# Kernel optimization log

Measured on AMD Instinct MI355X. Metric: run time of the kernel, lower is better.

The kernel has to match this reference:

```python
import jax, jax.numpy as jnp
import numpy as np

B, S, D, E = 8, 1024, 768, 8
F = 4 * D  # 3072


def setup_inputs() -> dict:
    key = jax.random.key(0)
    ks = jax.random.split(key, 5)
    scale = 0.02
    x = jax.random.normal(ks[0], (B, S, D), jnp.float32)
    gate_w = jax.random.normal(ks[1], (D, E), jnp.float32) * scale
    gate_b = jnp.zeros((E,), jnp.float32)
    w1 = jax.random.normal(ks[2], (E, D, F), jnp.float32) * scale
    b1 = jnp.zeros((E, F), jnp.float32)
    w2 = jax.random.normal(ks[3], (E, F, D), jnp.float32) * scale
    b2 = jnp.zeros((E, D), jnp.float32)
    return {"x": x, "gate_w": gate_w, "gate_b": gate_b,
            "w1": w1, "b1": b1, "w2": w2, "b2": b2}


def reference(x, gate_w, gate_b, w1, b1, w2, b2):
    # x: [B, S, D] -> tokens [T, D]
    orig_shape = x.shape
    xt = x.reshape(-1, x.shape[-1])  # [T, D]
    gates = jax.nn.softmax(xt @ gate_w + gate_b, axis=-1)  # [T, E]
    # original takes topk(k=2) but only uses indices[:, 0] == argmax (top-1)
    expert_idx = jnp.argmax(gates, axis=-1)  # [T]
    # NOTE: original does NOT scale expert output by gate probability.
    out = jnp.zeros_like(xt)
    n_experts = w1.shape[0]
    for e in range(n_experts):  # small fixed expert loop
        h = jax.nn.gelu(xt @ w1[e] + b1[e], approximate=False)  # [T, F]
        y = h @ w2[e] + b2[e]  # [T, D]
        out = jnp.where((expert_idx == e)[:, None], y, out)
    return out.reshape(orig_shape)
```

## Files before the change

### kernel.cpp

```cpp
#include <hip/hip_runtime.h>
#include <hip/hip_bf16.h>
#include <cstdint>
#include <cstddef>

static constexpr int T_TOK = 8192;
static constexpr int D_DIM = 768;
static constexpr int E_NUM = 8;
static constexpr int F_DIM = 3072;
static constexpr int MAX_TILES = 72;

typedef __attribute__((ext_vector_type(8))) short short8;
typedef __attribute__((ext_vector_type(4))) float floatx4;
typedef __attribute__((ext_vector_type(8))) unsigned short ushort8v;

__device__ __forceinline__ void async16(const void* g, void* l) {
  __builtin_amdgcn_global_load_lds(
      (const __attribute__((address_space(1))) unsigned int*)g,
      (__attribute__((address_space(3))) unsigned int*)l, 16, 0, 0);
}

__device__ __forceinline__ float gelu_fast(float v) {
  float s = v * (1.5957691f + 0.071354813f * v * v);
  return v / (1.0f + __expf(-s));
}

__global__ __launch_bounds__(256)
void gate_kernel(const float* __restrict__ x, const float* __restrict__ gw,
                 const float* __restrict__ gb, int* __restrict__ expert_idx,
                 __hip_bfloat16* __restrict__ xb) {
  int gid = blockIdx.x * blockDim.x + threadIdx.x;
  int tok = gid >> 6;
  int lane = threadIdx.x & 63;
  if (tok >= T_TOK) return;
  const float* xr = x + (size_t)tok * D_DIM;
  __hip_bfloat16* xbr = xb + (size_t)tok * D_DIM;
  float acc[8];
#pragma unroll
  for (int e = 0; e < 8; e++) acc[e] = 0.f;
#pragma unroll
  for (int i = 0; i < D_DIM / 64; i++) {
    int d = lane + i * 64;
    float v = xr[d];
    xbr[d] = __float2bfloat16(v);
    const float4* g4 = (const float4*)(gw + (size_t)d * 8);
    float4 a = g4[0], b = g4[1];
    acc[0] += v * a.x; acc[1] += v * a.y; acc[2] += v * a.z; acc[3] += v * a.w;
    acc[4] += v * b.x; acc[5] += v * b.y; acc[6] += v * b.z; acc[7] += v * b.w;
  }
#pragma unroll
  for (int e = 0; e < 8; e++) {
#pragma unroll
    for (int o = 32; o > 0; o >>= 1) acc[e] += __shfl_xor(acc[e], o, 64);
  }
  if (lane == 0) {
    int best = 0;
    float bv = acc[0] + gb[0];
#pragma unroll
    for (int e = 1; e < 8; e++) {
      float v = acc[e] + gb[e];
      if (v > bv) { bv = v; best = e; }
    }
    expert_idx[tok] = best;
  }
}

__global__ __launch_bounds__(256)
void count_kernel(const int* __restrict__ expert_idx, int* __restrict__ counts) {
  __shared__ int h[E_NUM];
  if (threadIdx.x < E_NUM) h[threadIdx.x] = 0;
  __syncthreads();
  int t = blockIdx.x * blockDim.x + threadIdx.x;
  if (t < T_TOK) atomicAdd(&h[expert_idx[t]], 1);
  __syncthreads();
  if (threadIdx.x < E_NUM && h[threadIdx.x] > 0)
    atomicAdd(&counts[threadIdx.x], h[threadIdx.x]);
}

__global__ void offsets_kernel(const int* __restrict__ counts, int* __restrict__ offs,
                               int* __restrict__ meta) {
  if (threadIdx.x == 0) {
    int s = 0, tc = 0;
    for (int e = 0; e < E_NUM; e++) {
      offs[e] = s;
      int cnt = counts[e];
      for (int m = 0; m * 128 < cnt; m++) {
        meta[1 + tc] = e;
        meta[1 + MAX_TILES + tc] = m;
        tc++;
      }
      s += cnt;
    }
    offs[E_NUM] = s;
    meta[0] = tc;
  }
}

__global__ __launch_bounds__(256)
void scatter_kernel(const int* __restrict__ expert_idx, const int* __restrict__ offs,
                    int* __restrict__ fill, int* __restrict__ perm) {
  __shared__ int lcnt[E_NUM];
  __shared__ int lbase[E_NUM];
  if (threadIdx.x < E_NUM) lcnt[threadIdx.x] = 0;
  __syncthreads();
  int t = blockIdx.x * blockDim.x + threadIdx.x;
  int e = -1, rank = 0;
  if (t < T_TOK) {
    e = expert_idx[t];
    rank = atomicAdd(&lcnt[e], 1);
  }
  __syncthreads();
  if (threadIdx.x < E_NUM)
    lbase[threadIdx.x] = (lcnt[threadIdx.x] > 0)
                           ? atomicAdd(&fill[threadIdx.x], lcnt[threadIdx.x]) : 0;
  __syncthreads();
  if (t < T_TOK) perm[offs[e] + lbase[e] + rank] = t;
}

__global__ __launch_bounds__(256)
void transpose_bf16(const float* __restrict__ in, __hip_bfloat16* __restrict__ out,
                    int R, int C) {
  __shared__ float t[64][65];
  const float* src = in + (size_t)blockIdx.z * R * C;
  __hip_bfloat16* dst = out + (size_t)blockIdx.z * R * C;
  int r0 = blockIdx.y * 64, c0 = blockIdx.x * 64;
  int tx = threadIdx.x & 15;
  int ty = threadIdx.x >> 4;
#pragma unroll
  for (int p = 0; p < 4; p++) {
    int r = ty + p * 16;
    float4 v = *(const float4*)&src[(size_t)(r0 + r) * C + c0 + tx * 4];
    t[tx * 4 + 0][r] = v.x; t[tx * 4 + 1][r] = v.y;
    t[tx * 4 + 2][r] = v.z; t[tx * 4 + 3][r] = v.w;
  }
  __syncthreads();
  int j = threadIdx.x & 7;
#pragma unroll
  for (int p = 0; p < 2; p++) {
    int cc = (threadIdx.x >> 3) + p * 32;
    __align__(16) __hip_bfloat16 tmp[8];
#pragma unroll
    for (int i = 0; i < 8; i++) tmp[i] = __float2bfloat16(t[cc][j * 8 + i]);
    *(ushort8v*)&dst[(size_t)(c0 + cc) * R + r0 + j * 8] = *(const ushort8v*)tmp;
  }
}

__global__ __launch_bounds__(256)
void moe_gemm1(const __hip_bfloat16* __restrict__ A,
               const __hip_bfloat16* __restrict__ Bt,
               const float* __restrict__ bias,
               const int* __restrict__ meta,
               const int* __restrict__ offs,
               const int* __restrict__ perm,
               __hip_bfloat16* __restrict__ H) {
  constexpr int K = D_DIM, N = F_DIM;
  int g = blockIdx.x;
  int xcd = g & 7;
  int j = g >> 3;
  int mt = xcd * 9 + (j % 9);
  int nt = j / 9;
  if (mt >= meta[0]) return;
  int e = meta[1 + mt];
  int m0 = meta[1 + MAX_TILES + mt] * 128;
  int off = offs[e], cnt = offs[e + 1] - off;
  int n0 = nt * 128;

  __shared__ __align__(16) __hip_bfloat16 As[2 * 128 * 32];
  __shared__ __align__(16) __hip_bfloat16 Bs[2 * 128 * 32];

  int tid = threadIdx.x, lane = tid & 63, w = tid >> 6;
  int lr0 = w * 32 + (lane >> 2), lr1 = lr0 + 16;
  int ch = (lane & 3) ^ ((lane >> 3) & 3);

  int r0 = m0 + lr0; if (r0 > cnt - 1) r0 = cnt - 1;
  int r1 = m0 + lr1; if (r1 > cnt - 1) r1 = cnt - 1;
  const __hip_bfloat16* a0 = A + (size_t)perm[off + r0] * K + ch * 8;
  const __hip_bfloat16* a1 = A + (size_t)perm[off + r1] * K + ch * 8;
  const __hip_bfloat16* Bbase = Bt + ((size_t)e * N + n0) * K;
  const __hip_bfloat16* bp0 = Bbase + (size_t)lr0 * K + ch * 8;
  const __hip_bfloat16* bp1 = Bbase + (size_t)lr1 * K + ch * 8;

  int wr = (w >> 1) * 64, wc = (w & 1) * 64;
  int mrow = lane & 15, cq = lane >> 4;
  int aoff[4], boff[4];
#pragma unroll
  for (int i = 0; i < 4; i++) {
    int rr = wr + i * 16 + mrow;
    aoff[i] = rr * 32 + ((cq ^ ((rr >> 1) & 3)) * 8);
    int rb = wc + i * 16 + mrow;
    boff[i] = rb * 32 + ((cq ^ ((rb >> 1) & 3)) * 8);
  }

  floatx4 acc[4][4];
#pragma unroll
  for (int i = 0; i < 4; i++)
#pragma unroll
    for (int jj = 0; jj < 4; jj++) acc[i][jj] = (floatx4){0.f, 0.f, 0.f, 0.f};

  for (int kk = 0; kk < K; kk += 64) {
    __syncthreads();
#pragma unroll
    for (int ks = 0; ks < 2; ks++) {
      int ko = kk + ks * 32;
      async16(a0 + ko, &As[ks * 4096 + (w * 32) * 32]);
      async16(a1 + ko, &As[ks * 4096 + (w * 32 + 16) * 32]);
      async16(bp0 + ko, &Bs[ks * 4096 + (w * 32) * 32]);
      async16(bp1 + ko, &Bs[ks * 4096 + (w * 32 + 16) * 32]);
    }
    __syncthreads();
#pragma unroll
    for (int ks = 0; ks < 2; ks++) {
      short8 af[4], bf[4];
#pragma unroll
      for (int i = 0; i < 4; i++) af[i] = *(const short8*)&As[ks * 4096 + aoff[i]];
#pragma unroll
      for (int i = 0; i < 4; i++) bf[i] = *(const short8*)&Bs[ks * 4096 + boff[i]];
#pragma unroll
      for (int mi = 0; mi < 4; mi++)
#pragma unroll
        for (int ni = 0; ni < 4; ni++)
          acc[mi][ni] = __builtin_amdgcn_mfma_f32_16x16x32_bf16(af[mi], bf[ni], acc[mi][ni], 0, 0, 0);
    }
  }

#pragma unroll
  for (int mi = 0; mi < 4; mi++) {
    int rowl = wr + mi * 16 + (lane >> 4) * 4;
#pragma unroll
    for (int ni = 0; ni < 4; ni++) {
      int col = n0 + wc + ni * 16 + (lane & 15);
      float bia = bias[(size_t)e * N + col];
#pragma unroll
      for (int r = 0; r < 4; r++) {
        int gm = m0 + rowl + r;
        if (gm < cnt)
          H[(size_t)(off + gm) * N + col] = __float2bfloat16(gelu_fast(acc[mi][ni][r] + bia));
      }
    }
  }
}

__global__ __launch_bounds__(256)
void moe_gemm2(const __hip_bfloat16* __restrict__ A,
               const __hip_bfloat16* __restrict__ Bt,
               const float* __restrict__ bias,
               const int* __restrict__ meta,
               const int* __restrict__ offs,
               const int* __restrict__ perm,
               float* __restrict__ Out) {
  constexpr int K = F_DIM, N = D_DIM;
  int g = blockIdx.x;
  int xcd = g & 7;
  int j = g >> 3;
  int mt = xcd * 9 + (j % 9);
  int nt = j / 9;
  if (mt >= meta[0]) return;
  int e = meta[1 + mt];
  int m0 = meta[1 + MAX_TILES + mt] * 128;
  int off = offs[e], cnt = offs[e + 1] - off;
  int n0 = nt * 64;

  __shared__ __align__(16) __hip_bfloat16 As[2 * 128 * 32];
  __shared__ __align__(16) __hip_bfloat16 Bs[2 * 64 * 32];

  int tid = threadIdx.x, lane = tid & 63, w = tid >> 6;
  int lr0 = w * 32 + (lane >> 2), lr1 = lr0 + 16;
  int ch = (lane & 3) ^ ((lane >> 3) & 3);

  int r0 = m0 + lr0; if (r0 > cnt - 1) r0 = cnt - 1;
  int r1 = m0 + lr1; if (r1 > cnt - 1) r1 = cnt - 1;
  const __hip_bfloat16* a0 = A + (size_t)(off + r0) * K + ch * 8;
  const __hip_bfloat16* a1 = A + (size_t)(off + r1) * K + ch * 8;
  int br = w * 16 + (lane >> 2);
  const __hip_bfloat16* bp0 = Bt + ((size_t)e * N + n0 + br) * K + ch * 8;

  int mrow = lane & 15, cq = lane >> 4;
  int aoff[2], boff[4];
#pragma unroll
  for (int i = 0; i < 2; i++) {
    int rr = w * 32 + i * 16 + mrow;
    aoff[i] = rr * 32 + ((cq ^ ((rr >> 1) & 3)) * 8);
  }
#pragma unroll
  for (int i = 0; i < 4; i++) {
    int rb = i * 16 + mrow;
    boff[i] = rb * 32 + ((cq ^ ((rb >> 1) & 3)) * 8);
  }

  floatx4 acc[2][4];
#pragma unroll
  for (int i = 0; i < 2; i++)
#pragma unroll
    for (int jj = 0; jj < 4; jj++) acc[i][jj] = (floatx4){0.f, 0.f, 0.f, 0.f};

  for (int kk = 0; kk < K; kk += 64) {
    __syncthreads();
#pragma unroll
    for (int ks = 0; ks < 2; ks++) {
      int ko = kk + ks * 32;
      async16(a0 + ko, &As[ks * 4096 + (w * 32) * 32]);
      async16(a1 + ko, &As[ks * 4096 + (w * 32 + 16) * 32]);
      async16(bp0 + ko, &Bs[ks * 2048 + (w * 16) * 32]);
    }
    __syncthreads();
#pragma unroll
    for (int ks = 0; ks < 2; ks++) {
      short8 af[2], bf[4];
#pragma unroll
      for (int i = 0; i < 2; i++) af[i] = *(const short8*)&As[ks * 4096 + aoff[i]];
#pragma unroll
      for (int i = 0; i < 4; i++) bf[i] = *(const short8*)&Bs[ks * 2048 + boff[i]];
#pragma unroll
      for (int mi = 0; mi < 2; mi++)
#pragma unroll
        for (int ni = 0; ni < 4; ni++)
          acc[mi][ni] = __builtin_amdgcn_mfma_f32_16x16x32_bf16(af[mi], bf[ni], acc[mi][ni], 0, 0, 0);
    }
  }

#pragma unroll
  for (int mi = 0; mi < 2; mi++) {
    int rowl = w * 32 + mi * 16 + (lane >> 4) * 4;
#pragma unroll
    for (int ni = 0; ni < 4; ni++) {
      int col = n0 + ni * 16 + (lane & 15);
      float bia = bias[(size_t)e * N + col];
#pragma unroll
      for (int r = 0; r < 4; r++) {
        int gm = m0 + rowl + r;
        if (gm < cnt)
          Out[(size_t)perm[off + gm] * N + col] = acc[mi][ni][r] + bia;
      }
    }
  }
}

extern "C" void kernel_launch(void* const* d_in, const int* in_sizes, int n_in,
                              void* d_out, int out_size, void* d_ws, size_t ws_size,
                              hipStream_t stream) {
  const float* x  = (const float*)d_in[0];
  const float* gw = (const float*)d_in[1];
  const float* gb = (const float*)d_in[2];
  const float* w1 = (const float*)d_in[3];
  const float* b1 = (const float*)d_in[4];
  const float* w2 = (const float*)d_in[5];
  const float* b2 = (const float*)d_in[6];
  float* out = (float*)d_out;

  char* ws = (char*)d_ws;
  int* counts = (int*)(ws + 0);
  int* fill   = (int*)(ws + 32);
  int* offs   = (int*)(ws + 64);
  int* meta   = (int*)(ws + 128);
  int* eidx   = (int*)(ws + 1024);
  int* perm   = (int*)(ws + 1024 + 4 * T_TOK);
  size_t off = 1024 + 8 * (size_t)T_TOK;
  __hip_bfloat16* xb  = (__hip_bfloat16*)(ws + off); off += (size_t)T_TOK * D_DIM * 2;
  __hip_bfloat16* w1t = (__hip_bfloat16*)(ws + off); off += (size_t)E_NUM * D_DIM * F_DIM * 2;
  __hip_bfloat16* w2t = (__hip_bfloat16*)(ws + off); off += (size_t)E_NUM * D_DIM * F_DIM * 2;
  __hip_bfloat16* H   = (__hip_bfloat16*)(ws + off); off += (size_t)T_TOK * F_DIM * 2;

  hipMemsetAsync(d_ws, 0, 64, stream);
  gate_kernel<<<T_TOK / 4, 256, 0, stream>>>(x, gw, gb, eidx, xb);
  count_kernel<<<T_TOK / 256, 256, 0, stream>>>(eidx, counts);
  offsets_kernel<<<1, 64, 0, stream>>>(counts, offs, meta);
  scatter_kernel<<<T_TOK / 256, 256, 0, stream>>>(eidx, offs, fill, perm);
  transpose_bf16<<<dim3(F_DIM / 64, D_DIM / 64, E_NUM), 256, 0, stream>>>(w1, w1t, D_DIM, F_DIM);
  transpose_bf16<<<dim3(D_DIM / 64, F_DIM / 64, E_NUM), 256, 0, stream>>>(w2, w2t, F_DIM, D_DIM);
  moe_gemm1<<<8 * 9 * (F_DIM / 128), 256, 0, stream>>>(xb, w1t, b1, meta, offs, perm, H);
  moe_gemm2<<<8 * 9 * (D_DIM / 64), 256, 0, stream>>>(H, w2t, b2, meta, offs, perm, out);
}
```

Before: 379.9 us.

## Double-buffer LDS tiles in a unified templated MoE GEMM with 128x128 tiles

Merges both expert GEMMs into one templated kernel that double-buffers LDS, issuing async global-to-LDS loads for the next K-step while MFMAs run on the current one, with explicit vmcnt waits and barriers. The second GEMM now uses 128-wide N tiles instead of 64, halving its grid and raising per-block reuse of the A tile. The aim is to hide global load latency that was previously exposed between two syncthreads. In exchange, LDS use doubles to 64KB per block, which may reduce occupancy, and the second GEMM has fewer blocks to spread across CUs.

```diff
diff --git a/kernel.cpp b/kernel.cpp
--- a/kernel.cpp
+++ b/kernel.cpp
@@ -144,15 +144,15 @@
   }
 }
 
-__global__ __launch_bounds__(256)
-void moe_gemm1(const __hip_bfloat16* __restrict__ A,
-               const __hip_bfloat16* __restrict__ Bt,
-               const float* __restrict__ bias,
-               const int* __restrict__ meta,
-               const int* __restrict__ offs,
-               const int* __restrict__ perm,
-               __hip_bfloat16* __restrict__ H) {
-  constexpr int K = D_DIM, N = F_DIM;
+template<int K, int N, bool FIRST>
+__global__ __launch_bounds__(256)
+void moe_gemm(const __hip_bfloat16* __restrict__ A,
+              const __hip_bfloat16* __restrict__ Bt,
+              const float* __restrict__ bias,
+              const int* __restrict__ meta,
+              const int* __restrict__ offs,
+              const int* __restrict__ perm,
+              void* __restrict__ OutP) {
   int g = blockIdx.x;
   int xcd = g & 7;
   int j = g >> 3;
@@ -164,8 +164,8 @@
   int off = offs[e], cnt = offs[e + 1] - off;
   int n0 = nt * 128;
 
-  __shared__ __align__(16) __hip_bfloat16 As[2 * 128 * 32];
-  __shared__ __align__(16) __hip_bfloat16 Bs[2 * 128 * 32];
+  __shared__ __align__(16) __hip_bfloat16 As[2 * 8192];
+  __shared__ __align__(16) __hip_bfloat16 Bs[2 * 8192];
 
   int tid = threadIdx.x, lane = tid & 63, w = tid >> 6;
   int lr0 = w * 32 + (lane >> 2), lr1 = lr0 + 16;
@@ -173,8 +173,15 @@
 
   int r0 = m0 + lr0; if (r0 > cnt - 1) r0 = cnt - 1;
   int r1 = m0 + lr1; if (r1 > cnt - 1) r1 = cnt - 1;
-  const __hip_bfloat16* a0 = A + (size_t)perm[off + r0] * K + ch * 8;
-  const __hip_bfloat16* a1 = A + (size_t)perm[off + r1] * K + ch * 8;
+  const __hip_bfloat16* a0;
+  const __hip_bfloat16* a1;
+  if constexpr (FIRST) {
+    a0 = A + (size_t)perm[off + r0] * K + ch * 8;
+    a1 = A + (size_t)perm[off + r1] * K + ch * 8;
+  } else {
+    a0 = A + (size_t)(off + r0) * K + ch * 8;
+    a1 = A + (size_t)(off + r1) * K + ch * 8;
+  }
   const __hip_bfloat16* Bbase = Bt + ((size_t)e * N + n0) * K;
   const __hip_bfloat16* bp0 = Bbase + (size_t)lr0 * K + ch * 8;
   const __hip_bfloat16* bp1 = Bbase + (size_t)lr1 * K + ch * 8;
@@ -190,36 +197,54 @@
     boff[i] = rb * 32 + ((cq ^ ((rb >> 1) & 3)) * 8);
   }
 
-  floatx4 acc[4][4];
-#pragma unroll
-  for (int i = 0; i < 4; i++)
-#pragma unroll
-    for (int jj = 0; jj < 4; jj++) acc[i][jj] = (floatx4){0.f, 0.f, 0.f, 0.f};
-
-  for (int kk = 0; kk < K; kk += 64) {
-    __syncthreads();
+  auto stage = [&](int buf, int kk) {
 #pragma unroll
     for (int ks = 0; ks < 2; ks++) {
       int ko = kk + ks * 32;
-      async16(a0 + ko, &As[ks * 4096 + (w * 32) * 32]);
-      async16(a1 + ko, &As[ks * 4096 + (w * 32 + 16) * 32]);
-      async16(bp0 + ko, &Bs[ks * 4096 + (w * 32) * 32]);
-      async16(bp1 + ko, &Bs[ks * 4096 + (w * 32 + 16) * 32]);
-    }
-    __syncthreads();
+      __hip_bfloat16* la = &As[buf * 8192 + ks * 4096];
+      __hip_bfloat16* lb = &Bs[buf * 8192 + ks * 4096];
+      async16(a0 + ko, la + (w * 32) * 32);
+      async16(a1 + ko, la + (w * 32 + 16) * 32);
+      async16(bp0 + ko, lb + (w * 32) * 32);
+      async16(bp1 + ko, lb + (w * 32 + 16) * 32);
+    }
+  };
+
+  floatx4 acc[4][4];
+#pragma unroll
+  for (int i = 0; i < 4; i++)
+#pragma unroll
+    for (int jj = 0; jj < 4; jj++) acc[i][jj] = (floatx4){0.f, 0.f, 0.f, 0.f};
+
+  constexpr int NT = K / 64;
+  stage(0, 0);
+  int p = 0;
+  for (int t = 0; t < NT; ++t) {
+    if (t + 1 < NT) {
+      stage(p ^ 1, (t + 1) * 64);
+      asm volatile("s_waitcnt vmcnt(8)" ::: "memory");
+    } else {
+      asm volatile("s_waitcnt vmcnt(0)" ::: "memory");
+    }
+    __builtin_amdgcn_s_barrier();
+    __builtin_amdgcn_sched_barrier(0);
 #pragma unroll
     for (int ks = 0; ks < 2; ks++) {
-      short8 af[4], bf[4];
-#pragma unroll
-      for (int i = 0; i < 4; i++) af[i] = *(const short8*)&As[ks * 4096 + aoff[i]];
-#pragma unroll
-      for (int i = 0; i < 4; i++) bf[i] = *(const short8*)&Bs[ks * 4096 + boff[i]];
+      int lb = p * 8192 + ks * 4096;
+      short8 af[4], bfv[4];
+#pragma unroll
+      for (int i = 0; i < 4; i++) af[i] = *(const short8*)&As[lb + aoff[i]];
+#pragma unroll
+      for (int i = 0; i < 4; i++) bfv[i] = *(const short8*)&Bs[lb + boff[i]];
 #pragma unroll
       for (int mi = 0; mi < 4; mi++)
 #pragma unroll
         for (int ni = 0; ni < 4; ni++)
-          acc[mi][ni] = __builtin_amdgcn_mfma_f32_16x16x32_bf16(af[mi], bf[ni], acc[mi][ni], 0, 0, 0);
-    }
+          acc[mi][ni] = __builtin_amdgcn_mfma_f32_16x16x32_bf16(af[mi], bfv[ni], acc[mi][ni], 0, 0, 0);
+    }
+    __builtin_amdgcn_sched_barrier(0);
+    __builtin_amdgcn_s_barrier();
+    p ^= 1;
   }
 
 #pragma unroll
@@ -232,103 +257,14 @@
 #pragma unroll
       for (int r = 0; r < 4; r++) {
         int gm = m0 + rowl + r;
-        if (gm < cnt)
-          H[(size_t)(off + gm) * N + col] = __float2bfloat16(gelu_fast(acc[mi][ni][r] + bia));
-      }
-    }
-  }
-}
-
-__global__ __launch_bounds__(256)
-void moe_gemm2(const __hip_bfloat16* __restrict__ A,
-               const __hip_bfloat16* __restrict__ Bt,
-               const float* __restrict__ bias,
-               const int* __restrict__ meta,
-               const int* __restrict__ offs,
-               const int* __restrict__ perm,
-               float* __restrict__ Out) {
-  constexpr int K = F_DIM, N = D_DIM;
-  int g = blockIdx.x;
-  int xcd = g & 7;
-  int j = g >> 3;
-  int mt = xcd * 9 + (j % 9);
-  int nt = j / 9;
-  if (mt >= meta[0]) return;
-  int e = meta[1 + mt];
-  int m0 = meta[1 + MAX_TILES + mt] * 128;
-  int off = offs[e], cnt = offs[e + 1] - off;
-  int n0 = nt * 64;
-
-  __shared__ __align__(16) __hip_bfloat16 As[2 * 128 * 32];
-  __shared__ __align__(16) __hip_bfloat16 Bs[2 * 64 * 32];
-
-  int tid = threadIdx.x, lane = tid & 63, w = tid >> 6;
-  int lr0 = w * 32 + (lane >> 2), lr1 = lr0 + 16;
-  int ch = (lane & 3) ^ ((lane >> 3) & 3);
-
-  int r0 = m0 + lr0; if (r0 > cnt - 1) r0 = cnt - 1;
-  int r1 = m0 + lr1; if (r1 > cnt - 1) r1 = cnt - 1;
-  const __hip_bfloat16* a0 = A + (size_t)(off + r0) * K + ch * 8;
-  const __hip_bfloat16* a1 = A + (size_t)(off + r1) * K + ch * 8;
-  int br = w * 16 + (lane >> 2);
-  const __hip_bfloat16* bp0 = Bt + ((size_t)e * N + n0 + br) * K + ch * 8;
-
-  int mrow = lane & 15, cq = lane >> 4;
-  int aoff[2], boff[4];
-#pragma unroll
-  for (int i = 0; i < 2; i++) {
-    int rr = w * 32 + i * 16 + mrow;
-    aoff[i] = rr * 32 + ((cq ^ ((rr >> 1) & 3)) * 8);
-  }
-#pragma unroll
-  for (int i = 0; i < 4; i++) {
-    int rb = i * 16 + mrow;
-    boff[i] = rb * 32 + ((cq ^ ((rb >> 1) & 3)) * 8);
-  }
-
-  floatx4 acc[2][4];
-#pragma unroll
-  for (int i = 0; i < 2; i++)
-#pragma unroll
-    for (int jj = 0; jj < 4; jj++) acc[i][jj] = (floatx4){0.f, 0.f, 0.f, 0.f};
-
-  for (int kk = 0; kk < K; kk += 64) {
-    __syncthreads();
-#pragma unroll
-    for (int ks = 0; ks < 2; ks++) {
-      int ko = kk + ks * 32;
-      async16(a0 + ko, &As[ks * 4096 + (w * 32) * 32]);
-      async16(a1 + ko, &As[ks * 4096 + (w * 32 + 16) * 32]);
-      async16(bp0 + ko, &Bs[ks * 2048 + (w * 16) * 32]);
-    }
-    __syncthreads();
-#pragma unroll
-    for (int ks = 0; ks < 2; ks++) {
-      short8 af[2], bf[4];
-#pragma unroll
-      for (int i = 0; i < 2; i++) af[i] = *(const short8*)&As[ks * 4096 + aoff[i]];
-#pragma unroll
-      for (int i = 0; i < 4; i++) bf[i] = *(const short8*)&Bs[ks * 2048 + boff[i]];
-#pragma unroll
-      for (int mi = 0; mi < 2; mi++)
-#pragma unroll
-        for (int ni = 0; ni < 4; ni++)
-          acc[mi][ni] = __builtin_amdgcn_mfma_f32_16x16x32_bf16(af[mi], bf[ni], acc[mi][ni], 0, 0, 0);
-    }
-  }
-
-#pragma unroll
-  for (int mi = 0; mi < 2; mi++) {
-    int rowl = w * 32 + mi * 16 + (lane >> 4) * 4;
-#pragma unroll
-    for (int ni = 0; ni < 4; ni++) {
-      int col = n0 + ni * 16 + (lane & 15);
-      float bia = bias[(size_t)e * N + col];
-#pragma unroll
-      for (int r = 0; r < 4; r++) {
-        int gm = m0 + rowl + r;
-        if (gm < cnt)
-          Out[(size_t)perm[off + gm] * N + col] = acc[mi][ni][r] + bia;
+        if (gm < cnt) {
+          if constexpr (FIRST) {
+            ((__hip_bfloat16*)OutP)[(size_t)(off + gm) * N + col] =
+                __float2bfloat16(gelu_fast(acc[mi][ni][r] + bia));
+          } else {
+            ((float*)OutP)[(size_t)perm[off + gm] * N + col] = acc[mi][ni][r] + bia;
+          }
+        }
       }
     }
   }
@@ -366,6 +302,8 @@
   scatter_kernel<<<T_TOK / 256, 256, 0, stream>>>(eidx, offs, fill, perm);
   transpose_bf16<<<dim3(F_DIM / 64, D_DIM / 64, E_NUM), 256, 0, stream>>>(w1, w1t, D_DIM, F_DIM);
   transpose_bf16<<<dim3(D_DIM / 64, F_DIM / 64, E_NUM), 256, 0, stream>>>(w2, w2t, F_DIM, D_DIM);
-  moe_gemm1<<<8 * 9 * (F_DIM / 128), 256, 0, stream>>>(xb, w1t, b1, meta, offs, perm, H);
-  moe_gemm2<<<8 * 9 * (D_DIM / 64), 256, 0, stream>>>(H, w2t, b2, meta, offs, perm, out);
-}
+  moe_gemm<D_DIM, F_DIM, true><<<8 * 9 * (F_DIM / 128), 256, 0, stream>>>(
+      xb, w1t, b1, meta, offs, perm, (void*)H);
+  moe_gemm<F_DIM, D_DIM, false><<<8 * 9 * (D_DIM / 128), 256, 0, stream>>>(
+      H, w2t, b2, meta, offs, perm, (void*)out);
+}
```

Measured after the change: 385.2 us. Within noise of the previous version (+1.4%).

## Triple-buffer gemm1 K-loop with async prefetch and fuse expert counting into gate

Applied to the files above, without the earlier changes.

The gemm1 K loop moves from a load-then-compute scheme, with two syncs per 64-wide step, to a three-slot ring of 32-wide stages. Loads are issued two stages ahead and gated by explicit vmcnt waits, so global-to-LDS transfers overlap MFMA work. Separately, per-block expert histogram counting moves into the gate kernel, which removes one kernel launch. The risks are a larger LDS footprint, and manual waitcnt values that depend on the compiler not issuing other vector memory ops in between.

```diff
diff --git a/kernel.cpp b/kernel.cpp
--- a/kernel.cpp
+++ b/kernel.cpp
@@ -27,11 +27,13 @@
 __global__ __launch_bounds__(256)
 void gate_kernel(const float* __restrict__ x, const float* __restrict__ gw,
                  const float* __restrict__ gb, int* __restrict__ expert_idx,
-                 __hip_bfloat16* __restrict__ xb) {
+                 __hip_bfloat16* __restrict__ xb, int* __restrict__ counts) {
+  __shared__ int h[E_NUM];
+  if (threadIdx.x < E_NUM) h[threadIdx.x] = 0;
+  __syncthreads();
   int gid = blockIdx.x * blockDim.x + threadIdx.x;
   int tok = gid >> 6;
   int lane = threadIdx.x & 63;
-  if (tok >= T_TOK) return;
   const float* xr = x + (size_t)tok * D_DIM;
   __hip_bfloat16* xbr = xb + (size_t)tok * D_DIM;
   float acc[8];
@@ -61,16 +63,8 @@
       if (v > bv) { bv = v; best = e; }
     }
     expert_idx[tok] = best;
-  }
-}
-
-__global__ __launch_bounds__(256)
-void count_kernel(const int* __restrict__ expert_idx, int* __restrict__ counts) {
-  __shared__ int h[E_NUM];
-  if (threadIdx.x < E_NUM) h[threadIdx.x] = 0;
-  __syncthreads();
-  int t = blockIdx.x * blockDim.x + threadIdx.x;
-  if (t < T_TOK) atomicAdd(&h[expert_idx[t]], 1);
+    atomicAdd(&h[best], 1);
+  }
   __syncthreads();
   if (threadIdx.x < E_NUM && h[threadIdx.x] > 0)
     atomicAdd(&counts[threadIdx.x], h[threadIdx.x]);
@@ -164,8 +158,8 @@
   int off = offs[e], cnt = offs[e + 1] - off;
   int n0 = nt * 128;
 
-  __shared__ __align__(16) __hip_bfloat16 As[2 * 128 * 32];
-  __shared__ __align__(16) __hip_bfloat16 Bs[2 * 128 * 32];
+  __shared__ __align__(16) __hip_bfloat16 As[3 * 4096];
+  __shared__ __align__(16) __hip_bfloat16 Bs[3 * 4096];
 
   int tid = threadIdx.x, lane = tid & 63, w = tid >> 6;
   int lr0 = w * 32 + (lane >> 2), lr1 = lr0 + 16;
@@ -190,36 +184,48 @@
     boff[i] = rb * 32 + ((cq ^ ((rb >> 1) & 3)) * 8);
   }
 
+  auto stage = [&](int slot, int ko) {
+    __hip_bfloat16* la = &As[slot * 4096];
+    __hip_bfloat16* lb = &Bs[slot * 4096];
+    async16(a0 + ko, la + (w * 32) * 32);
+    async16(a1 + ko, la + (w * 32 + 16) * 32);
+    async16(bp0 + ko, lb + (w * 32) * 32);
+    async16(bp1 + ko, lb + (w * 32 + 16) * 32);
+  };
+
   floatx4 acc[4][4];
 #pragma unroll
   for (int i = 0; i < 4; i++)
 #pragma unroll
     for (int jj = 0; jj < 4; jj++) acc[i][jj] = (floatx4){0.f, 0.f, 0.f, 0.f};
 
-  for (int kk = 0; kk < K; kk += 64) {
-    __syncthreads();
-#pragma unroll
-    for (int ks = 0; ks < 2; ks++) {
-      int ko = kk + ks * 32;
-      async16(a0 + ko, &As[ks * 4096 + (w * 32) * 32]);
-      async16(a1 + ko, &As[ks * 4096 + (w * 32 + 16) * 32]);
-      async16(bp0 + ko, &Bs[ks * 4096 + (w * 32) * 32]);
-      async16(bp1 + ko, &Bs[ks * 4096 + (w * 32 + 16) * 32]);
-    }
-    __syncthreads();
-#pragma unroll
-    for (int ks = 0; ks < 2; ks++) {
-      short8 af[4], bf[4];
-#pragma unroll
-      for (int i = 0; i < 4; i++) af[i] = *(const short8*)&As[ks * 4096 + aoff[i]];
-#pragma unroll
-      for (int i = 0; i < 4; i++) bf[i] = *(const short8*)&Bs[ks * 4096 + boff[i]];
-#pragma unroll
-      for (int mi = 0; mi < 4; mi++)
-#pragma unroll
-        for (int ni = 0; ni < 4; ni++)
-          acc[mi][ni] = __builtin_amdgcn_mfma_f32_16x16x32_bf16(af[mi], bf[ni], acc[mi][ni], 0, 0, 0);
-    }
+  constexpr int NT = K / 32;
+  stage(0, 0);
+  stage(1, 32);
+  for (int t = 0; t < NT; ++t) {
+    if (t + 2 < NT) {
+      stage((t + 2) % 3, (t + 2) * 32);
+      asm volatile("s_waitcnt vmcnt(8)" ::: "memory");
+    } else if (t + 1 < NT) {
+      asm volatile("s_waitcnt vmcnt(4)" ::: "memory");
+    } else {
+      asm volatile("s_waitcnt vmcnt(0)" ::: "memory");
+    }
+    __builtin_amdgcn_s_barrier();
+    __builtin_amdgcn_sched_barrier(0);
+    int lb = (t % 3) * 4096;
+    short8 af[4], bfv[4];
+#pragma unroll
+    for (int i = 0; i < 4; i++) af[i] = *(const short8*)&As[lb + aoff[i]];
+#pragma unroll
+    for (int i = 0; i < 4; i++) bfv[i] = *(const short8*)&Bs[lb + boff[i]];
+#pragma unroll
+    for (int mi = 0; mi < 4; mi++)
+#pragma unroll
+      for (int ni = 0; ni < 4; ni++)
+        acc[mi][ni] = __builtin_amdgcn_mfma_f32_16x16x32_bf16(af[mi], bfv[ni], acc[mi][ni], 0, 0, 0);
+    __builtin_amdgcn_sched_barrier(0);
+    __builtin_amdgcn_s_barrier();
   }
 
 #pragma unroll
@@ -360,8 +366,7 @@
   __hip_bfloat16* H   = (__hip_bfloat16*)(ws + off); off += (size_t)T_TOK * F_DIM * 2;
 
   hipMemsetAsync(d_ws, 0, 64, stream);
-  gate_kernel<<<T_TOK / 4, 256, 0, stream>>>(x, gw, gb, eidx, xb);
-  count_kernel<<<T_TOK / 256, 256, 0, stream>>>(eidx, counts);
+  gate_kernel<<<T_TOK / 4, 256, 0, stream>>>(x, gw, gb, eidx, xb, counts);
   offsets_kernel<<<1, 64, 0, stream>>>(counts, offs, meta);
   scatter_kernel<<<T_TOK / 256, 256, 0, stream>>>(eidx, offs, fill, perm);
   transpose_bf16<<<dim3(F_DIM / 64, D_DIM / 64, E_NUM), 256, 0, stream>>>(w1, w1t, D_DIM, F_DIM);
```

After: 398.4 us. +4.9%, slower.
